# Kernel optimization log

Hardware: AMD Instinct MI355X
Metric: run time of the kernel (lower is better)

## Reference

```python
import jax, jax.numpy as jnp
import numpy as np

N = 1024      # n_nodes
F = 64        # n_features
L = 64        # lookback_window (must equal F for U1 @ B to typecheck, as in the torch code)
NDF = 4       # n_data_features
NTF = 8       # n_time_features
FC1 = 1024
FC2 = 512
K = 2         # kernel_size
DIL = (2, 2)  # dilation_list
DELTA = 0.05
EPS = 1e-5


def _ln(x, g, b):
    mu = x.mean(-1, keepdims=True)
    v = ((x - mu) ** 2).mean(-1, keepdims=True)
    return (x - mu) / jnp.sqrt(v + EPS) * g + b


def _mlp2(x, W1, b1, g, bb, W2, b2):
    h = jax.nn.relu(_ln(x @ W1 + b1, g, bb))
    return h @ W2 + b2


def setup_inputs() -> dict:
    ks = jax.random.split(jax.random.key(0), 16)
    def rn(i, shape, s=1.0):
        return jax.random.normal(ks[i], shape, dtype=jnp.float32) * s
    z = lambda *s: jnp.zeros(s, jnp.float32)
    o = lambda *s: jnp.ones(s, jnp.float32)
    return {
        "observation": rn(0, (N, NDF, L)),
        "time_features": rn(1, (L, NTF)),
        "layer_initial": rn(2, (L, N)),
        "sW1": rn(3, (N, 256), N ** -0.5), "sb1": z(256), "s_ln_g": o(256), "s_ln_b": z(256),
        "sW2": rn(4, (256, N * F), 256 ** -0.5), "sb2": z(N * F),
        "tW1": rn(5, (NTF, 256), NTF ** -0.5), "tb1": z(256), "t_ln_g": o(256), "t_ln_b": z(256),
        "tW2": rn(6, (256, N * F), 256 ** -0.5), "tb2": z(N * F),
        "B": o(F, F),
        "fW1": rn(7, (N * NDF, FC1), (N * NDF) ** -0.5), "fb1": z(FC1), "f1g": o(FC1), "f1b": z(FC1),
        "fW2": rn(8, (FC1, FC2), FC1 ** -0.5), "fb2": z(FC2), "f2g": o(FC2), "f2b": z(FC2),
        "fW3": rn(9, (FC2, N * F), FC2 ** -0.5), "fb3": z(N * F),
        "Wf": rn(10, (K, F, F)), "Wb": rn(11, (K, F, F)), "bconv": rn(12, (F,)),
    }


def _forward(observation, time_features, layer_initial, sW1, sb1, s_ln_g, s_ln_b, sW2, sb2,
             tW1, tb1, t_ln_g, t_ln_b, tW2, tb2, B,
             fW1, fb1, f1g, f1b, fW2, fb2, f2g, f2b, fW3, fb3, Wf, Wb, bconv):
    # GraphConstructor node embedding; U[:, :, j] is (N, L)
    emb = _mlp2(layer_initial, sW1, sb1, s_ln_g, s_ln_b, sW2, sb2) \
        + _mlp2(time_features, tW1, tb1, t_ln_g, t_ln_b, tW2, tb2)   # (L, N*F)
    U = emb.reshape(L, N, F).transpose(1, 0, 2)                      # (N, L, F)
    Uf = jnp.moveaxis(U, 2, 0)                                       # (F, N, L) for feature-axis gathers

    def adj(aidx, bidx):
        # batched adjacency: softmax over rows of thresholded U1 B U2^T, then D^-1/2 A D^-1/2
        Ua, Ub = Uf[aidx], Uf[bidx]                                  # (M, N, L)
        S = jax.lax.stop_gradient(jnp.einsum('mnl,lp,mqp->mnq', Ua, B, Ub))  # .detach() in torch
        S = jnp.where(S >= DELTA, S, 0.0)
        A = jax.nn.softmax(S, axis=-1)
        dn = 1.0 / jnp.sqrt(A.sum(-1))                               # degree is diagonal -> sqrtm/inverse = elementwise
        return A * dn[:, :, None] * dn[:, None, :]

    # fully_connected: observation (N, NDF, L) -> X (N, F, L)
    obs = observation.transpose(2, 0, 1).reshape(L, N * NDF)
    h = jax.nn.relu(_ln(obs @ fW1 + fb1, f1g, f1b))
    h = jax.nn.relu(_ln(h @ fW2 + fb2, f2g, f2b))
    X = (h @ fW3 + fb3).reshape(L, N, F).transpose(1, 2, 0)          # (N, F, L)

    gamma = 1
    outs = []
    for d in DIL:
        length = X.shape[-1]
        ts = np.arange(d - 1, length, d)                             # t with (t+1) % d == 0, static
        Z = jnp.zeros((ts.size, N, F), X.dtype)
        for k in range(K):
            tk = ts - k                                              # >= 0 since K <= min(DIL)
            Xk = X[:, :, tk]                                         # (N, F, M)
            A1 = adj((gamma * tk) % L, (gamma * ts) % L)             # pair (idx - k*gamma, idx)
            A2 = adj((gamma * ts) % L, (gamma * tk) % L)             # pair (idx, idx - k*gamma)
            msg = jnp.einsum('mnq,qfm->mnf', A1, Xk) @ Wf[k] \
                + jnp.einsum('mnq,qfm->mnf', A2, Xk) @ Wb[k] + bconv
            Z = Z + jnp.tanh(msg)
        X = jnp.moveaxis(Z, 0, 2)                                    # (N, F, M) becomes next layer input
        outs.append(X[:, :, -1])
        gamma *= d
    return jnp.stack(outs)                                           # (len(DIL), N, F)


def reference(observation, time_features, layer_initial, sW1, sb1, s_ln_g, s_ln_b, sW2, sb2,
              tW1, tb1, t_ln_g, t_ln_b, tW2, tb2, B,
              fW1, fb1, f1g, f1b, fW2, fb2, f2g, f2b, fW3, fb3, Wf, Wb, bconv):
    return _forward(observation, time_features, layer_initial, sW1, sb1, s_ln_g, s_ln_b, sW2, sb2,
                    tW1, tb1, t_ln_g, t_ln_b, tW2, tb2, B,
                    fW1, fb1, f1g, f1b, fW2, fb2, f2g, f2b, fW3, fb3, Wf, Wb, bconv)
```

## Files before the change

### kernel.cpp

```cpp
#include <hip/hip_runtime.h>
#include <cstddef>

#define EPS_C   1e-5f
#define DELTA_C 0.05f
#define NS      8

struct Pairs { int a[6]; int b[6]; int t[6]; };


template<int K>
__device__ __forceinline__ void head_body(
    const float* __restrict__ A, const float* __restrict__ W1,
    const float* __restrict__ b1, const float* __restrict__ g,
    const float* __restrict__ bb, float* __restrict__ H,
    float* As, float* rs, float* rs2, int row, int j)
{
  for (int i = j; i < K; i += 256) As[i] = A[row * K + i];
  __syncthreads();

  float a0 = 0.f, a1 = 0.f, a2 = 0.f, a3 = 0.f;
  const float* __restrict__ Wp = W1 + j;
#pragma unroll 2
  for (int c = 0; c < K; c += 8) {
    float w0 = Wp[(size_t)(c + 0) * 256];
    float w1 = Wp[(size_t)(c + 1) * 256];
    float w2 = Wp[(size_t)(c + 2) * 256];
    float w3 = Wp[(size_t)(c + 3) * 256];
    float w4 = Wp[(size_t)(c + 4) * 256];
    float w5 = Wp[(size_t)(c + 5) * 256];
    float w6 = Wp[(size_t)(c + 6) * 256];
    float w7 = Wp[(size_t)(c + 7) * 256];
    a0 += As[c + 0] * w0 + As[c + 4] * w4;
    a1 += As[c + 1] * w1 + As[c + 5] * w5;
    a2 += As[c + 2] * w2 + As[c + 6] * w6;
    a3 += As[c + 3] * w3 + As[c + 7] * w7;
  }
  float acc = ((a0 + a1) + (a2 + a3)) + b1[j];

  rs[j] = acc; rs2[j] = acc * acc;
  __syncthreads();
  for (int st = 128; st > 0; st >>= 1) {
    if (j < st) { rs[j] += rs[j + st]; rs2[j] += rs2[j + st]; }
    __syncthreads();
  }
  float mu  = rs[0] * (1.f / 256.f);
  float var = rs2[0] * (1.f / 256.f) - mu * mu;
  float y = (acc - mu) * rsqrtf(var + EPS_C) * g[j] + bb[j];
  H[row * 256 + j] = fmaxf(y, 0.f);
}

template<int MODE>
__device__ __forceinline__ void skinny_body(
    const float* __restrict__ A, const float* __restrict__ W,
    float* __restrict__ part, int K, int N, int bid, int tid,
    float (*ARs)[64])
{
  int jblocks = N >> 8;
  int jb = bid % jblocks;
  int kc = bid / jblocks;
  int k0 = kc << 6;
  {
    int c = tid >> 6, i = tid & 63;
    int k = k0 + i;
    float v;
    if (MODE == 0) v = A[c * K + k];
    else { int n = k >> 2, df = k & 3; v = A[n * 256 + df * 64 + 60 + c]; }
    ARs[c][i] = v;
  }
  __syncthreads();
  int j = (jb << 8) + tid;
  float acc0 = 0.f, acc1 = 0.f, acc2 = 0.f, acc3 = 0.f;
#pragma unroll
  for (int kk = 0; kk < 64; kk += 16) {
    float w[16];
#pragma unroll
    for (int u = 0; u < 16; ++u) w[u] = W[(size_t)(k0 + kk + u) * N + j];
#pragma unroll
    for (int u = 0; u < 16; ++u) {
      acc0 += ARs[0][kk + u] * w[u];
      acc1 += ARs[1][kk + u] * w[u];
      acc2 += ARs[2][kk + u] * w[u];
      acc3 += ARs[3][kk + u] * w[u];
    }
  }
  part[(size_t)(kc * 4 + 0) * N + j] = acc0;
  part[(size_t)(kc * 4 + 1) * N + j] = acc1;
  part[(size_t)(kc * 4 + 2) * N + j] = acc2;
  part[(size_t)(kc * 4 + 3) * N + j] = acc3;
}

template<int N_, int PARTS>
__device__ __forceinline__ void red_body(
    const float* __restrict__ part, const float* __restrict__ bias,
    const float* __restrict__ g, const float* __restrict__ bb,
    float* __restrict__ out, int c, int tid, float* rs, float* rs2)
{
  constexpr int PER = N_ >> 8;
  float x[PER];
  float s = 0.f, s2 = 0.f;
#pragma unroll
  for (int i = 0; i < PER; ++i) {
    int j = (i << 8) + tid;
    float v = bias[j];
#pragma unroll 8
    for (int p = 0; p < PARTS; ++p) v += part[(size_t)(p * 4 + c) * N_ + j];
    x[i] = v; s += v; s2 += v * v;
  }
  rs[tid] = s; rs2[tid] = s2;
  __syncthreads();
  for (int st = 128; st > 0; st >>= 1) {
    if (tid < st) { rs[tid] += rs[tid + st]; rs2[tid] += rs2[tid + st]; }
    __syncthreads();
  }
  float mu  = rs[0] / (float)N_;
  float var = rs2[0] / (float)N_ - mu * mu;
  float inv = rsqrtf(var + EPS_C);
#pragma unroll
  for (int i = 0; i < PER; ++i) {
    int j = (i << 8) + tid;
    out[c * N_ + j] = fmaxf((x[i] - mu) * inv * g[j] + bb[j], 0.f);
  }
}


__global__ __launch_bounds__(256) void k1_heads_skinny(
    const float* __restrict__ layer_initial, const float* __restrict__ sW1,
    const float* __restrict__ sb1, const float* __restrict__ s_g,
    const float* __restrict__ s_b, float* __restrict__ Hs,
    const float* __restrict__ time_features, const float* __restrict__ tW1,
    const float* __restrict__ tb1, const float* __restrict__ t_g,
    const float* __restrict__ t_b, float* __restrict__ Ht,
    const float* __restrict__ observation, const float* __restrict__ fW1,
    float* __restrict__ part1)
{
  __shared__ float As[1024];
  __shared__ float rs[256], rs2[256];
  __shared__ float ARs[4][64];
  int bid = blockIdx.x, j = threadIdx.x;
  if (bid < 64) {
    head_body<1024>(layer_initial, sW1, sb1, s_g, s_b, Hs, As, rs, rs2, bid, j);
  } else if (bid < 128) {
    head_body<8>(time_features, tW1, tb1, t_g, t_b, Ht, As, rs, rs2, bid - 64, j);
  } else {
    skinny_body<1>(observation, fW1, part1, 4096, 1024, bid - 128, j, ARs);
  }
}

__global__ __launch_bounds__(256) void k2_emb_red1(
    const float* __restrict__ Hs, const float* __restrict__ Ht,
    const float* __restrict__ sW2, const float* __restrict__ sb2,
    const float* __restrict__ tW2, const float* __restrict__ tb2,
    float* __restrict__ Vs,
    const float* __restrict__ part1, const float* __restrict__ fb1,
    const float* __restrict__ f1g, const float* __restrict__ f1b,
    float* __restrict__ h1)
{
  __shared__ float wS[256][4], wT[256][4];
  int tid = threadIdx.x;
  if (blockIdx.x < 1024) {
    int n = blockIdx.x;
    int l = tid >> 2, c = tid & 3;
    {
      size_t base = (size_t)tid * 65536 + (size_t)n * 64 + 60;
      float4 a = *(const float4*)&sW2[base];
      float4 t4 = *(const float4*)&tW2[base];
      wS[tid][0] = a.x;  wS[tid][1] = a.y;  wS[tid][2] = a.z;  wS[tid][3] = a.w;
      wT[tid][0] = t4.x; wT[tid][1] = t4.y; wT[tid][2] = t4.z; wT[tid][3] = t4.w;
    }
    __syncthreads();
    const float* __restrict__ hs = Hs + l * 256;
    const float* __restrict__ ht = Ht + l * 256;
    float acc = 0.f;
    for (int k = 0; k < 256; k += 8) {
#pragma unroll
      for (int u = 0; u < 8; ++u)
        acc += hs[k + u] * wS[k + u][c] + ht[k + u] * wT[k + u][c];
    }
    int jj = n * 64 + 60 + c;
    Vs[(size_t)c * 65536 + (size_t)n * 64 + l] = acc + sb2[jj] + tb2[jj];
  } else {
    red_body<1024, 64>(part1, fb1, f1g, f1b, h1, blockIdx.x - 1024, tid,
                       &wS[0][0], &wT[0][0]);
  }
}

__global__ __launch_bounds__(256) void k3_vab_skinny(
    const float* __restrict__ Vs, const float* __restrict__ Bmat,
    float* __restrict__ VaBt, float* __restrict__ VsT,
    const float* __restrict__ h1, const float* __restrict__ fW2,
    float* __restrict__ part2)
{
  __shared__ float Va[64][65], Bs[64][65];
  int tid = threadIdx.x;
  if (blockIdx.x < 64) {
    int c = blockIdx.x >> 4, nb = blockIdx.x & 15;
    int n0 = nb << 6;
    int rg = tid >> 4, cg = tid & 15;
#pragma unroll
    for (int i = 0; i < 4; ++i) {
      int flat = i * 1024 + tid * 4;
      int rr = flat >> 6, cc = flat & 63;
      float4 v = *(const float4*)&Vs[(size_t)c * 65536 + (size_t)(n0 + rr) * 64 + cc];
      Va[rr][cc] = v.x; Va[rr][cc+1] = v.y; Va[rr][cc+2] = v.z; Va[rr][cc+3] = v.w;
      float4 w = *(const float4*)&Bmat[flat];
      Bs[rr][cc] = w.x; Bs[rr][cc+1] = w.y; Bs[rr][cc+2] = w.z; Bs[rr][cc+3] = w.w;
    }
    __syncthreads();
#pragma unroll
    for (int i = 0; i < 4; ++i) {
      int flat = i * 1024 + tid * 4;
      int l = flat >> 6, nn = flat & 63;
      float4 st = { Va[nn][l], Va[nn+1][l], Va[nn+2][l], Va[nn+3][l] };
      *(float4*)&VsT[(size_t)c * 65536 + (size_t)l * 1024 + n0 + nn] = st;
    }
    float acc[4][4];
#pragma unroll
    for (int i = 0; i < 4; ++i)
#pragma unroll
      for (int j = 0; j < 4; ++j) acc[i][j] = 0.f;
#pragma unroll 4
    for (int l = 0; l < 64; ++l) {
      float av[4], bv[4];
#pragma unroll
      for (int i = 0; i < 4; ++i) av[i] = Va[rg * 4 + i][l];
#pragma unroll
      for (int j = 0; j < 4; ++j) bv[j] = Bs[l][cg * 4 + j];
#pragma unroll
      for (int i = 0; i < 4; ++i)
#pragma unroll
        for (int j = 0; j < 4; ++j) acc[i][j] += av[i] * bv[j];
    }
#pragma unroll
    for (int j = 0; j < 4; ++j) {
      float4 st = { acc[0][j], acc[1][j], acc[2][j], acc[3][j] };
      *(float4*)&VaBt[(size_t)c * 65536 + (size_t)(cg * 4 + j) * 1024 + n0 + rg * 4] = st;
    }
  } else {
    skinny_body<0>(h1, fW2, part2, 1024, 512, blockIdx.x - 64, tid,
                   (float(*)[64])&Va[0][0]);
  }
}

__global__ __launch_bounds__(256) void big_w3b(
    const float* __restrict__ part2, const float* __restrict__ fb2,
    const float* __restrict__ f2g, const float* __restrict__ f2b,
    const float* __restrict__ fW3, const float* __restrict__ fb3,
    float* __restrict__ Xr)
{
  int tid = threadIdx.x;
  __shared__ float h2s[2048];
  __shared__ float sm[4][128];
  {
    int c = tid >> 6, lane = tid & 63;
    float v[8]; float s = 0.f, s2 = 0.f;
#pragma unroll
    for (int k = 0; k < 8; ++k) {
      int j = lane + k * 64;
      float x = fb2[j];
#pragma unroll
      for (int p = 0; p < 16; ++p) x += part2[(size_t)(p * 4 + c) * 512 + j];
      v[k] = x; s += x; s2 += x * x;
    }
#pragma unroll
    for (int off = 1; off < 64; off <<= 1) {
      s += __shfl_xor(s, off); s2 += __shfl_xor(s2, off);
    }
    float mu = s * (1.f / 512.f);
    float var = s2 * (1.f / 512.f) - mu * mu;
    float inv = rsqrtf(var + EPS_C);
#pragma unroll
    for (int k = 0; k < 8; ++k) {
      int j = lane + k * 64;
      h2s[c * 512 + j] = fmaxf((v[k] - mu) * inv * f2g[j] + f2b[j], 0.f);
    }
  }
  __syncthreads();

  int col = tid & 127, ks = tid >> 7;
  int j = blockIdx.x * 128 + col;
  int kbase = ks << 8;
  float acc0 = 0.f, acc1 = 0.f, acc2 = 0.f, acc3 = 0.f;
  for (int k0 = 0; k0 < 256; k0 += 16) {
    float w[16];
#pragma unroll
    for (int u = 0; u < 16; ++u) w[u] = fW3[(size_t)(kbase + k0 + u) * 65536 + j];
#pragma unroll
    for (int u = 0; u < 16; ++u) {
      int k = kbase + k0 + u;
      acc0 += h2s[k]        * w[u];
      acc1 += h2s[512 + k]  * w[u];
      acc2 += h2s[1024 + k] * w[u];
      acc3 += h2s[1536 + k] * w[u];
    }
  }
  if (ks) { sm[0][col] = acc0; sm[1][col] = acc1; sm[2][col] = acc2; sm[3][col] = acc3; }
  __syncthreads();
  if (!ks) {
    float b = fb3[j];
    Xr[j]            = acc0 + sm[0][col] + b;
    Xr[65536 + j]    = acc1 + sm[1][col] + b;
    Xr[131072 + j]   = acc2 + sm[2][col] + b;
    Xr[196608 + j]   = acc3 + sm[3][col] + b;
  }
}

__global__ __launch_bounds__(256) void attn_partial(
    const float* __restrict__ VaBt, const float* __restrict__ VsT,
    const float* __restrict__ Xbase, float* __restrict__ Pl,
    float* __restrict__ ml, Pairs pr, int slotBase)
{
  int pi  = blockIdx.x >> 7;
  int rem = blockIdx.x & 127;
  int nb  = rem >> 3;
  int s   = rem & 7;
  int n0  = nb << 6;
  int tid = threadIdx.x;
  int rg = tid >> 4, cg = tid & 15;
  int rg4 = rg * 4, cg4 = cg * 4;
  int a = pr.a[pi], b = pr.b[pi], t = pr.t[pi];

  __shared__ __align__(16) float VaT[64][68];
  __shared__ __align__(16) float VbT[64][68];
  __shared__ __align__(16) float Xs[64][68];
  float (*St)[68] = VbT;

#pragma unroll
  for (int i = 0; i < 4; ++i) {
    int flat = i * 1024 + tid * 4;
    int p = flat >> 6, nn = flat & 63;
    float4 v = *(const float4*)&VaBt[(size_t)a * 65536 + (size_t)p * 1024 + n0 + nn];
    *(float4*)&VaT[p][nn] = v;
  }
  float m_run[4], l_run[4];
#pragma unroll
  for (int i = 0; i < 4; ++i) { m_run[i] = -1e30f; l_run[i] = 0.f; }
  float P[4][4];
#pragma unroll
  for (int i = 0; i < 4; ++i)
#pragma unroll
    for (int j = 0; j < 4; ++j) P[i][j] = 0.f;
  __syncthreads();

  for (int ti = 0; ti < 2; ++ti) {
    int q0 = (s << 7) + (ti << 6);
    if (ti) __syncthreads();
#pragma unroll
    for (int i = 0; i < 4; ++i) {
      int flat = i * 1024 + tid * 4;
      int p = flat >> 6, qq = flat & 63;
      float4 v = *(const float4*)&VsT[(size_t)b * 65536 + (size_t)p * 1024 + q0 + qq];
      *(float4*)&VbT[p][qq] = v;
      float4 x = *(const float4*)&Xbase[(size_t)t * 65536 + (size_t)(q0 + p) * 64 + qq];
      *(float4*)&Xs[p][qq] = x;
    }
    __syncthreads();
    float sa[4][4];
#pragma unroll
    for (int i = 0; i < 4; ++i)
#pragma unroll
      for (int j = 0; j < 4; ++j) sa[i][j] = 0.f;
#pragma unroll 4
    for (int p = 0; p < 64; ++p) {
      float av[4], bv[4];
      *(float4*)av = *(const float4*)&VaT[p][rg4];
      *(float4*)bv = *(const float4*)&VbT[p][cg4];
#pragma unroll
      for (int i = 0; i < 4; ++i)
#pragma unroll
        for (int j = 0; j < 4; ++j) sa[i][j] += av[i] * bv[j];
    }
    float scv[4];
#pragma unroll
    for (int i = 0; i < 4; ++i) {
#pragma unroll
      for (int j = 0; j < 4; ++j) sa[i][j] = (sa[i][j] >= DELTA_C) ? sa[i][j] : 0.f;
      float tm = fmaxf(fmaxf(sa[i][0], sa[i][1]), fmaxf(sa[i][2], sa[i][3]));
      tm = fmaxf(tm, __shfl_xor(tm, 1));
      tm = fmaxf(tm, __shfl_xor(tm, 2));
      tm = fmaxf(tm, __shfl_xor(tm, 4));
      tm = fmaxf(tm, __shfl_xor(tm, 8));
      float mnew = fmaxf(m_run[i], tm);
      float sc = __expf(m_run[i] - mnew);
      float ssum = 0.f;
#pragma unroll
      for (int j = 0; j < 4; ++j) {
        float e = __expf(sa[i][j] - mnew);
        sa[i][j] = e;
        ssum += e;
      }
      ssum += __shfl_xor(ssum, 1);
      ssum += __shfl_xor(ssum, 2);
      ssum += __shfl_xor(ssum, 4);
      ssum += __shfl_xor(ssum, 8);
      l_run[i] = l_run[i] * sc + ssum;
      m_run[i] = mnew;
      scv[i] = sc;
    }
    __syncthreads();
#pragma unroll
    for (int i = 0; i < 4; ++i) {
      float4 e4 = { sa[i][0], sa[i][1], sa[i][2], sa[i][3] };
      *(float4*)&St[rg4 + i][cg4] = e4;
    }
    __syncthreads();
#pragma unroll
    for (int i = 0; i < 4; ++i)
#pragma unroll
      for (int j = 0; j < 4; ++j) P[i][j] *= scv[i];
#pragma unroll 2
    for (int q4 = 0; q4 < 64; q4 += 4) {
      float4 ev[4], xv[4];
#pragma unroll
      for (int i = 0; i < 4; ++i) ev[i] = *(const float4*)&St[rg4 + i][q4];
#pragma unroll
      for (int u = 0; u < 4; ++u) xv[u] = *(const float4*)&Xs[q4 + u][cg4];
#pragma unroll
      for (int i = 0; i < 4; ++i) {
        const float* e = &ev[i].x;
#pragma unroll
        for (int u = 0; u < 4; ++u) {
          const float* x = &xv[u].x;
#pragma unroll
          for (int j = 0; j < 4; ++j) P[i][j] += e[u] * x[j];
        }
      }
    }
  }
  size_t base = (size_t)((slotBase + pi) * 16 + nb) * NS + s;
  float* pp = Pl + base * 4096;
#pragma unroll
  for (int i = 0; i < 4; ++i) {
    float4 st = { P[i][0], P[i][1], P[i][2], P[i][3] };
    *(float4*)&pp[(size_t)(rg4 + i) * 64 + cg4] = st;
  }
  if ((tid & 15) == 0) {
    float* mlp = ml + base * 128;
#pragma unroll
    for (int i = 0; i < 4; ++i) {
      mlp[rg4 + i]      = m_run[i];
      mlp[64 + rg4 + i] = l_run[i];
    }
  }
}

__global__ __launch_bounds__(256) void merge_partial(
    const float* __restrict__ Pl, const float* __restrict__ ml,
    const float* __restrict__ Wf, const float* __restrict__ Wb,
    int slotBase, float* __restrict__ Gp)
{
  int mm = blockIdx.x / 48;
  int rem = blockIdx.x % 48;
  int nb = rem / 3, inst = rem % 3;
  int n0 = nb << 6;
  int tid = threadIdx.x;
  int rg = tid >> 4, cg = tid & 15;
  int rg4 = rg * 4, cg4 = cg * 4;
  int r = tid >> 2, sub = tid & 3;

  __shared__ __align__(16) float PtT[64][68];
  __shared__ __align__(16) float Wt[64][68];

  int slot = slotBase + mm * 3 + inst;
  size_t base = (size_t)(slot * 16 + nb) * NS;
  const float* mlp = ml + base * 128;
  float mg = -1e30f;
#pragma unroll
  for (int s2 = 0; s2 < NS; ++s2) mg = fmaxf(mg, mlp[s2 * 128 + r]);
  float acc[16];
#pragma unroll
  for (int u = 0; u < 16; ++u) acc[u] = 0.f;
  float lg = 0.f;
#pragma unroll
  for (int s2 = 0; s2 < NS; ++s2) {
    float f = __expf(mlp[s2 * 128 + r] - mg);
    lg += f * mlp[s2 * 128 + 64 + r];
    const float4* ps = (const float4*)(Pl + (base + s2) * 4096 + r * 64 + sub * 16);
#pragma unroll
    for (int u = 0; u < 4; ++u) {
      float4 v = ps[u];
      acc[u*4+0] += f * v.x; acc[u*4+1] += f * v.y;
      acc[u*4+2] += f * v.z; acc[u*4+3] += f * v.w;
    }
  }
  float inv = 1.f / lg;
#pragma unroll
  for (int u = 0; u < 16; ++u) PtT[sub * 16 + u][r] = acc[u] * inv;
  for (int i = tid; i < 4096; i += 256) {
    int rr = i >> 6, cc = i & 63;
    float w;
    if (inst == 0)      w = Wf[i] + Wb[i];
    else if (inst == 1) w = Wf[4096 + i];
    else                w = Wb[4096 + i];
    Wt[rr][cc] = w;
  }
  __syncthreads();
  float g2[4][4];
#pragma unroll
  for (int i = 0; i < 4; ++i)
#pragma unroll
    for (int j = 0; j < 4; ++j) g2[i][j] = 0.f;
#pragma unroll 4
  for (int ff = 0; ff < 64; ++ff) {
    float p[4], w[4];
    *(float4*)p = *(const float4*)&PtT[ff][rg4];
    *(float4*)w = *(const float4*)&Wt[ff][cg4];
#pragma unroll
    for (int i = 0; i < 4; ++i)
#pragma unroll
      for (int j = 0; j < 4; ++j) g2[i][j] += p[i] * w[j];
  }
#pragma unroll
  for (int i = 0; i < 4; ++i) {
    float4 st = { g2[i][0], g2[i][1], g2[i][2], g2[i][3] };
    *(float4*)&Gp[(size_t)(mm * 3 + inst) * 65536 + (size_t)(n0 + rg4 + i) * 64 + cg4] = st;
  }
}

__global__ __launch_bounds__(256) void finalize_z(
    const float* __restrict__ Gp, const float* __restrict__ bconv,
    float* __restrict__ dst0, float* __restrict__ dst1, float* __restrict__ extra1)
{
  int mm = blockIdx.x >> 4;
  int nb = blockIdx.x & 15;
  int tid = threadIdx.x;
  size_t tileOff = (size_t)(nb << 6) * 64;
  const float* g0 = Gp + (size_t)(mm * 3 + 0) * 65536 + tileOff;
  const float* g1 = Gp + (size_t)(mm * 3 + 1) * 65536 + tileOff;
  const float* g2 = Gp + (size_t)(mm * 3 + 2) * 65536 + tileOff;
  float* dst = (mm == 0) ? dst0 : dst1;
  for (int i = tid * 4; i < 4096; i += 1024) {
    float4 a = *(const float4*)&g0[i];
    float4 b = *(const float4*)&g1[i];
    float4 c = *(const float4*)&g2[i];
    int col = i & 63;
    float4 z;
    z.x = tanhf(a.x + bconv[col+0]) + tanhf(b.x + c.x + bconv[col+0]);
    z.y = tanhf(a.y + bconv[col+1]) + tanhf(b.y + c.y + bconv[col+1]);
    z.z = tanhf(a.z + bconv[col+2]) + tanhf(b.z + c.z + bconv[col+2]);
    z.w = tanhf(a.w + bconv[col+3]) + tanhf(b.w + c.w + bconv[col+3]);
    *(float4*)&dst[tileOff + i] = z;
    if (mm == 1 && extra1) *(float4*)&extra1[tileOff + i] = z;
  }
}

extern "C" void kernel_launch(void* const* d_in, const int* in_sizes, int n_in,
                              void* d_out, int out_size, void* d_ws, size_t ws_size,
                              hipStream_t stream)
{
  const float* observation   = (const float*)d_in[0];
  const float* time_features = (const float*)d_in[1];
  const float* layer_initial = (const float*)d_in[2];
  const float* sW1   = (const float*)d_in[3];
  const float* sb1   = (const float*)d_in[4];
  const float* s_ln_g = (const float*)d_in[5];
  const float* s_ln_b = (const float*)d_in[6];
  const float* sW2   = (const float*)d_in[7];
  const float* sb2   = (const float*)d_in[8];
  const float* tW1   = (const float*)d_in[9];
  const float* tb1   = (const float*)d_in[10];
  const float* t_ln_g = (const float*)d_in[11];
  const float* t_ln_b = (const float*)d_in[12];
  const float* tW2   = (const float*)d_in[13];
  const float* tb2   = (const float*)d_in[14];
  const float* Bmat  = (const float*)d_in[15];
  const float* fW1   = (const float*)d_in[16];
  const float* fb1   = (const float*)d_in[17];
  const float* f1g   = (const float*)d_in[18];
  const float* f1b   = (const float*)d_in[19];
  const float* fW2   = (const float*)d_in[20];
  const float* fb2   = (const float*)d_in[21];
  const float* f2g   = (const float*)d_in[22];
  const float* f2b   = (const float*)d_in[23];
  const float* fW3   = (const float*)d_in[24];
  const float* fb3   = (const float*)d_in[25];
  const float* Wf    = (const float*)d_in[26];
  const float* Wb    = (const float*)d_in[27];
  const float* bconv = (const float*)d_in[28];
  float* out = (float*)d_out;

  float* ws    = (float*)d_ws;
  float* Hs    = ws;
  float* Ht    = Hs    + 16384;
  float* Vs    = Ht    + 16384;
  float* VsT   = Vs    + 262144;
  float* VaBt  = VsT   + 262144;
  float* part1 = VaBt  + 262144;
  float* part2 = part1 + 262144;
  float* h1    = part2 + 32768;
  float* Xr    = h1    + 4096;
  float* Pl    = Xr    + 262144;
  float* ml    = Pl    + 4718592;
  float* Z1    = ml    + 147456;
  float* Gp    = Z1    + 131072;

  k1_heads_skinny<<<384, 256, 0, stream>>>(
      layer_initial, sW1, sb1, s_ln_g, s_ln_b, Hs,
      time_features, tW1, tb1, t_ln_g, t_ln_b, Ht,
      observation, fW1, part1);
  k2_emb_red1<<<1028, 256, 0, stream>>>(
      Hs, Ht, sW2, sb2, tW2, tb2, Vs,
      part1, fb1, f1g, f1b, h1);
  k3_vab_skinny<<<96, 256, 0, stream>>>(Vs, Bmat, VaBt, VsT, h1, fW2, part2);
  big_w3b<<<512, 256, 0, stream>>>(part2, fb2, f2g, f2b, fW3, fb3, Xr);

  Pairs pA;
  pA.a[0]=1; pA.b[0]=1; pA.t[0]=1;
  pA.a[1]=0; pA.b[1]=1; pA.t[1]=0;
  pA.a[2]=1; pA.b[2]=0; pA.t[2]=0;
  pA.a[3]=3; pA.b[3]=3; pA.t[3]=3;
  pA.a[4]=2; pA.b[4]=3; pA.t[4]=2;
  pA.a[5]=3; pA.b[5]=2; pA.t[5]=2;
  attn_partial<<<6 * 16 * NS, 256, 0, stream>>>(VaBt, VsT, Xr, Pl, ml, pA, 0);
  merge_partial<<<96, 256, 0, stream>>>(Pl, ml, Wf, Wb, 0, Gp);
  finalize_z<<<32, 256, 0, stream>>>(Gp, bconv, Z1, Z1 + 65536, out);

  Pairs pB;
  pB.a[0]=2; pB.b[0]=2; pB.t[0]=1;
  pB.a[1]=0; pB.b[1]=2; pB.t[1]=0;
  pB.a[2]=2; pB.b[2]=0; pB.t[2]=0;
  pB.a[3]=pB.a[4]=pB.a[5]=0; pB.b[3]=pB.b[4]=pB.b[5]=0; pB.t[3]=pB.t[4]=pB.t[5]=0;
  attn_partial<<<3 * 16 * NS, 256, 0, stream>>>(VaBt, VsT, Z1, Pl, ml, pB, 6);
  merge_partial<<<48, 256, 0, stream>>>(Pl, ml, Wf, Wb, 6, Gp);
  finalize_z<<<16, 256, 0, stream>>>(Gp, bconv, out + 65536, nullptr, nullptr);
}
```

Before: 177.7 us.

## Retile embedding GEMM over 4 nodes and raise split count for second attention

The embedding projection kernel now handles four nodes per block instead of one. It stages H transposed and W chunks in shared memory with register prefetch of the next chunk, so H reads are reused across nodes and the grid shrinks from 1024 to 256 blocks. The attention partial and merge kernels are templated on the split count. The second dilation layer now uses 16 splits instead of 8, which gives 768 blocks instead of 384 so the device is better filled, and its partials go to separate buffers. The cost is more partials to merge and a longer serial chunk loop in the embedding blocks.

```diff
diff --git a/kernel.cpp b/kernel.cpp
--- a/kernel.cpp
+++ b/kernel.cpp
@@ -3,7 +3,6 @@
 
 #define EPS_C   1e-5f
 #define DELTA_C 0.05f
-#define NS      8
 
 struct Pairs { int a[6]; int b[6]; int t[6]; };
 
@@ -155,32 +154,68 @@
     const float* __restrict__ f1g, const float* __restrict__ f1b,
     float* __restrict__ h1)
 {
-  __shared__ float wS[256][4], wT[256][4];
+  __shared__ __align__(16) float HcT[64][68];
+  __shared__ __align__(16) float Wc[64][20];
   int tid = threadIdx.x;
-  if (blockIdx.x < 1024) {
-    int n = blockIdx.x;
-    int l = tid >> 2, c = tid & 3;
+  if (blockIdx.x < 256) {
+    int n0 = blockIdx.x * 4;
+    int lq = tid >> 4, jc = tid & 15;
+    int nn = n0 + (jc >> 2), cc = jc & 3;
+    int kkw = tid >> 2, nloc = tid & 3;
+
+    float4 hr[4]; float4 wr;
     {
-      size_t base = (size_t)tid * 65536 + (size_t)n * 64 + 60;
-      float4 a = *(const float4*)&sW2[base];
-      float4 t4 = *(const float4*)&tW2[base];
-      wS[tid][0] = a.x;  wS[tid][1] = a.y;  wS[tid][2] = a.z;  wS[tid][3] = a.w;
-      wT[tid][0] = t4.x; wT[tid][1] = t4.y; wT[tid][2] = t4.z; wT[tid][3] = t4.w;
-    }
-    __syncthreads();
-    const float* __restrict__ hs = Hs + l * 256;
-    const float* __restrict__ ht = Ht + l * 256;
-    float acc = 0.f;
-    for (int k = 0; k < 256; k += 8) {
-#pragma unroll
-      for (int u = 0; u < 8; ++u)
-        acc += hs[k + u] * wS[k + u][c] + ht[k + u] * wT[k + u][c];
-    }
-    int jj = n * 64 + 60 + c;
-    Vs[(size_t)c * 65536 + (size_t)n * 64 + l] = acc + sb2[jj] + tb2[jj];
+      const float* __restrict__ Hsrc = Hs;
+      const float* __restrict__ Wsrc = sW2;
+#pragma unroll
+      for (int i = 0; i < 4; ++i) {
+        int flat = i * 1024 + tid * 4;
+        int l = flat >> 6, kk = flat & 63;
+        hr[i] = *(const float4*)&Hsrc[l * 256 + kk];
+      }
+      wr = *(const float4*)&Wsrc[(size_t)kkw * 65536 + (size_t)(n0 + nloc) * 64 + 60];
+    }
+    float acc0 = 0.f, acc1 = 0.f, acc2 = 0.f, acc3 = 0.f;
+    for (int ch = 0; ch < 8; ++ch) {
+      __syncthreads();
+#pragma unroll
+      for (int i = 0; i < 4; ++i) {
+        int flat = i * 1024 + tid * 4;
+        int l = flat >> 6, kk = flat & 63;
+        HcT[kk + 0][l] = hr[i].x;
+        HcT[kk + 1][l] = hr[i].y;
+        HcT[kk + 2][l] = hr[i].z;
+        HcT[kk + 3][l] = hr[i].w;
+      }
+      *(float4*)&Wc[kkw][nloc * 4] = wr;
+      __syncthreads();
+      if (ch < 7) {
+        int nc2 = ch + 1;
+        const float* __restrict__ Hsrc = (nc2 < 4) ? Hs : Ht;
+        const float* __restrict__ Wsrc = (nc2 < 4) ? sW2 : tW2;
+        int kl = (nc2 & 3) << 6;
+#pragma unroll
+        for (int i = 0; i < 4; ++i) {
+          int flat = i * 1024 + tid * 4;
+          int l = flat >> 6, kk = flat & 63;
+          hr[i] = *(const float4*)&Hsrc[l * 256 + kl + kk];
+        }
+        wr = *(const float4*)&Wsrc[(size_t)(kl + kkw) * 65536 + (size_t)(n0 + nloc) * 64 + 60];
+      }
+#pragma unroll 8
+      for (int kk = 0; kk < 64; ++kk) {
+        float4 av = *(const float4*)&HcT[kk][lq * 4];
+        float w = Wc[kk][jc];
+        acc0 += av.x * w; acc1 += av.y * w; acc2 += av.z * w; acc3 += av.w * w;
+      }
+    }
+    int jj = nn * 64 + 60 + cc;
+    float bias = sb2[jj] + tb2[jj];
+    float4 st = { acc0 + bias, acc1 + bias, acc2 + bias, acc3 + bias };
+    *(float4*)&Vs[(size_t)cc * 65536 + (size_t)nn * 64 + lq * 4] = st;
   } else {
-    red_body<1024, 64>(part1, fb1, f1g, f1b, h1, blockIdx.x - 1024, tid,
-                       &wS[0][0], &wT[0][0]);
+    red_body<1024, 64>(part1, fb1, f1g, f1b, h1, blockIdx.x - 256, tid,
+                       &HcT[0][0], &HcT[0][0] + 256);
   }
 }
 
@@ -304,15 +339,17 @@
   }
 }
 
+template<int NSPLIT>
 __global__ __launch_bounds__(256) void attn_partial(
     const float* __restrict__ VaBt, const float* __restrict__ VsT,
     const float* __restrict__ Xbase, float* __restrict__ Pl,
-    float* __restrict__ ml, Pairs pr, int slotBase)
-{
-  int pi  = blockIdx.x >> 7;
-  int rem = blockIdx.x & 127;
-  int nb  = rem >> 3;
-  int s   = rem & 7;
+    float* __restrict__ ml, Pairs pr)
+{
+  constexpr int TILES = 16 / NSPLIT;
+  int pi  = blockIdx.x / (16 * NSPLIT);
+  int rem = blockIdx.x % (16 * NSPLIT);
+  int nb  = rem / NSPLIT;
+  int s   = rem % NSPLIT;
   int n0  = nb << 6;
   int tid = threadIdx.x;
   int rg = tid >> 4, cg = tid & 15;
@@ -341,8 +378,8 @@
     for (int j = 0; j < 4; ++j) P[i][j] = 0.f;
   __syncthreads();
 
-  for (int ti = 0; ti < 2; ++ti) {
-    int q0 = (s << 7) + (ti << 6);
+  for (int ti = 0; ti < TILES; ++ti) {
+    int q0 = (s * TILES + ti) << 6;
     if (ti) __syncthreads();
 #pragma unroll
     for (int i = 0; i < 4; ++i) {
@@ -426,7 +463,7 @@
       }
     }
   }
-  size_t base = (size_t)((slotBase + pi) * 16 + nb) * NS + s;
+  size_t base = (size_t)((pi * 16 + nb) * NSPLIT + s);
   float* pp = Pl + base * 4096;
 #pragma unroll
   for (int i = 0; i < 4; ++i) {
@@ -443,10 +480,11 @@
   }
 }
 
+template<int NS_T>
 __global__ __launch_bounds__(256) void merge_partial(
     const float* __restrict__ Pl, const float* __restrict__ ml,
     const float* __restrict__ Wf, const float* __restrict__ Wb,
-    int slotBase, float* __restrict__ Gp)
+    float* __restrict__ Gp)
 {
   int mm = blockIdx.x / 48;
   int rem = blockIdx.x % 48;
@@ -460,18 +498,17 @@
   __shared__ __align__(16) float PtT[64][68];
   __shared__ __align__(16) float Wt[64][68];
 
-  int slot = slotBase + mm * 3 + inst;
-  size_t base = (size_t)(slot * 16 + nb) * NS;
+  size_t base = (size_t)((mm * 3 + inst) * 16 + nb) * NS_T;
   const float* mlp = ml + base * 128;
   float mg = -1e30f;
 #pragma unroll
-  for (int s2 = 0; s2 < NS; ++s2) mg = fmaxf(mg, mlp[s2 * 128 + r]);
+  for (int s2 = 0; s2 < NS_T; ++s2) mg = fmaxf(mg, mlp[s2 * 128 + r]);
   float acc[16];
 #pragma unroll
   for (int u = 0; u < 16; ++u) acc[u] = 0.f;
   float lg = 0.f;
 #pragma unroll
-  for (int s2 = 0; s2 < NS; ++s2) {
+  for (int s2 = 0; s2 < NS_T; ++s2) {
     float f = __expf(mlp[s2 * 128 + r] - mg);
     lg += f * mlp[s2 * 128 + 64 + r];
     const float4* ps = (const float4*)(Pl + (base + s2) * 4096 + r * 64 + sub * 16);
@@ -589,15 +626,17 @@
   float* h1    = part2 + 32768;
   float* Xr    = h1    + 4096;
   float* Pl    = Xr    + 262144;
-  float* ml    = Pl    + 4718592;
-  float* Z1    = ml    + 147456;
+  float* ml    = Pl    + 3145728;
+  float* Pl2   = ml    + 98304;
+  float* ml2   = Pl2   + 3145728;
+  float* Z1    = ml2   + 98304;
   float* Gp    = Z1    + 131072;
 
   k1_heads_skinny<<<384, 256, 0, stream>>>(
       layer_initial, sW1, sb1, s_ln_g, s_ln_b, Hs,
       time_features, tW1, tb1, t_ln_g, t_ln_b, Ht,
       observation, fW1, part1);
-  k2_emb_red1<<<1028, 256, 0, stream>>>(
+  k2_emb_red1<<<260, 256, 0, stream>>>(
       Hs, Ht, sW2, sb2, tW2, tb2, Vs,
       part1, fb1, f1g, f1b, h1);
   k3_vab_skinny<<<96, 256, 0, stream>>>(Vs, Bmat, VaBt, VsT, h1, fW2, part2);
@@ -610,8 +649,8 @@
   pA.a[3]=3; pA.b[3]=3; pA.t[3]=3;
   pA.a[4]=2; pA.b[4]=3; pA.t[4]=2;
   pA.a[5]=3; pA.b[5]=2; pA.t[5]=2;
-  attn_partial<<<6 * 16 * NS, 256, 0, stream>>>(VaBt, VsT, Xr, Pl, ml, pA, 0);
-  merge_partial<<<96, 256, 0, stream>>>(Pl, ml, Wf, Wb, 0, Gp);
+  attn_partial<8><<<6 * 16 * 8, 256, 0, stream>>>(VaBt, VsT, Xr, Pl, ml, pA);
+  merge_partial<8><<<96, 256, 0, stream>>>(Pl, ml, Wf, Wb, Gp);
   finalize_z<<<32, 256, 0, stream>>>(Gp, bconv, Z1, Z1 + 65536, out);
 
   Pairs pB;
@@ -619,7 +658,7 @@
   pB.a[1]=0; pB.b[1]=2; pB.t[1]=0;
   pB.a[2]=2; pB.b[2]=0; pB.t[2]=0;
   pB.a[3]=pB.a[4]=pB.a[5]=0; pB.b[3]=pB.b[4]=pB.b[5]=0; pB.t[3]=pB.t[4]=pB.t[5]=0;
-  attn_partial<<<3 * 16 * NS, 256, 0, stream>>>(VaBt, VsT, Z1, Pl, ml, pB, 6);
-  merge_partial<<<48, 256, 0, stream>>>(Pl, ml, Wf, Wb, 6, Gp);
+  attn_partial<16><<<3 * 16 * 16, 256, 0, stream>>>(VaBt, VsT, Z1, Pl2, ml2, pB);
+  merge_partial<16><<<48, 256, 0, stream>>>(Pl2, ml2, Wf, Wb, Gp);
   finalize_z<<<16, 256, 0, stream>>>(Gp, bconv, out + 65536, nullptr, nullptr);
 }
```

Result: faster. 164.0 us (-7.7%).
